# Kernel optimization log

Measured on AMD Instinct MI355X. Metric: run time of the kernel, lower is better.

## Reference

```python
import jax, jax.numpy as jnp
import numpy as np

N_NODES = 100000

def setup_inputs() -> dict:
    key = jax.random.key(0)
    k1, k2, k3, k4, k5 = jax.random.split(key, 5)
    E = 1600000
    feat = jax.random.normal(k1, (N_NODES, 128), dtype=jnp.float32)
    W = jax.random.normal(k2, (128, 32), dtype=jnp.float32) * 0.08  # ~xavier scale
    edge_w = jax.random.uniform(k3, (E,), dtype=jnp.float32)
    src = jax.random.randint(k4, (E,), 0, N_NODES, dtype=jnp.int32)
    dst = jax.random.randint(k5, (E,), 0, N_NODES, dtype=jnp.int32)
    return {"feat": feat, "W": W, "edge_w": edge_w, "src": src, "dst": dst}

def reference(feat, W, edge_w, src, dst):
    # linear transform: [N, in] @ [in, out] -> [N, out]
    h = feat @ W
    # gather source features per edge, scale by edge weight: u_mul_e
    m = h[src] * edge_w[:, None]  # [E, out]
    # sum messages at destination nodes
    rst = jax.ops.segment_sum(m, dst, num_segments=N_NODES)  # [N, out]
    return rst
```

## Files before the change

kernel.cpp:

```cpp
#include <hip/hip_runtime.h>
#include <hip/hip_fp16.h>

constexpr int N_IN    = 128;
constexpr int N_OUT   = 32;
constexpr int LOG_R   = 6;
constexpr int RANGE   = 1 << LOG_R;
constexpr int MAXNB   = 2048;
constexpr int NCC     = 256;
constexpr int PBLK    = 512;
constexpr int CHUNK_P = 2048;

union H4 { uint2 u; __half2 h2[2]; };
union H8 { uint4 u; __half2 h2[4]; };

__global__ __launch_bounds__(256) void gemm_h(
    const float* __restrict__ feat, const float* __restrict__ W,
    __half* __restrict__ h, int n)
{
    __shared__ float Ws[N_IN * N_OUT];
    for (int i = threadIdx.x; i < (N_IN * N_OUT) / 4; i += 256)
        reinterpret_cast<float4*>(Ws)[i] = reinterpret_cast<const float4*>(W)[i];
    __syncthreads();

    int gid = blockIdx.x * 256 + threadIdx.x;
    int row = gid >> 3;
    if (row >= n) return;
    int cg = (gid & 7) * 4;

    const float4* frow = reinterpret_cast<const float4*>(feat + (size_t)row * N_IN);
    float4 acc = make_float4(0.f, 0.f, 0.f, 0.f);
    #pragma unroll
    for (int k4 = 0; k4 < N_IN / 4; ++k4) {
        float4 f = frow[k4];
        int k = k4 * 4;
        float4 w0 = *reinterpret_cast<const float4*>(&Ws[(k + 0) * N_OUT + cg]);
        float4 w1 = *reinterpret_cast<const float4*>(&Ws[(k + 1) * N_OUT + cg]);
        float4 w2 = *reinterpret_cast<const float4*>(&Ws[(k + 2) * N_OUT + cg]);
        float4 w3 = *reinterpret_cast<const float4*>(&Ws[(k + 3) * N_OUT + cg]);
        acc.x += f.x * w0.x + f.y * w1.x + f.z * w2.x + f.w * w3.x;
        acc.y += f.x * w0.y + f.y * w1.y + f.z * w2.y + f.w * w3.y;
        acc.z += f.x * w0.z + f.y * w1.z + f.z * w2.z + f.w * w3.z;
        acc.w += f.x * w0.w + f.y * w1.w + f.z * w2.w + f.w * w3.w;
    }
    H4 v;
    v.h2[0] = __float22half2_rn(make_float2(acc.x, acc.y));
    v.h2[1] = __float22half2_rn(make_float2(acc.z, acc.w));
    *reinterpret_cast<uint2*>(h + (size_t)row * N_OUT + cg) = v.u;
}

__global__ __launch_bounds__(PBLK) void partition2_k(
    const int* __restrict__ src, const int* __restrict__ dst,
    const float* __restrict__ w, int* __restrict__ tbl,
    int2* __restrict__ sw, int E, int NB, int epc)
{
    __shared__ int hist[MAXNB];
    __shared__ int wscan[PBLK];

    const int c   = blockIdx.x;
    const int tid = threadIdx.x;
    const int e0  = c * epc;
    const int e1  = min(e0 + epc, E);
    const int m   = max(e1 - e0, 0);
    const int m4  = m & ~3;
    const int slots = (NB + PBLK - 1) / PBLK;

    for (int i = tid; i < NB; i += PBLK) hist[i] = 0;
    __syncthreads();

    for (int o = tid * 4; o < m4; o += PBLK * 4) {
        int4 dv = *reinterpret_cast<const int4*>(dst + e0 + o);
        atomicAdd(&hist[dv.x >> LOG_R], 1);
        atomicAdd(&hist[dv.y >> LOG_R], 1);
        atomicAdd(&hist[dv.z >> LOG_R], 1);
        atomicAdd(&hist[dv.w >> LOG_R], 1);
    }
    if (m4 + tid < m) atomicAdd(&hist[dst[e0 + m4 + tid] >> LOG_R], 1);
    __syncthreads();

    int tsum = 0;
    int base = tid * slots;
    for (int j = 0; j < slots; ++j) {
        int idx = base + j;
        if (idx < NB) tsum += hist[idx];
    }
    wscan[tid] = tsum;
    __syncthreads();
    for (int off = 1; off < PBLK; off <<= 1) {
        int x = (tid >= off) ? wscan[tid - off] : 0;
        __syncthreads();
        wscan[tid] += x;
        __syncthreads();
    }
    int run = wscan[tid] - tsum;
    __syncthreads();
    for (int j = 0; j < slots; ++j) {
        int idx = base + j;
        if (idx < NB) {
            int cval = hist[idx];
            tbl[(size_t)c * (NB + 1) + idx] = run;
            hist[idx] = run;
            run += cval;
        }
    }
    if (tid == 0) tbl[(size_t)c * (NB + 1) + NB] = m;
    __syncthreads();

    int2* outp = sw + (size_t)c * epc;
    for (int o = tid * 4; o < m4; o += PBLK * 4) {
        int4   sv = *reinterpret_cast<const int4*>(src + e0 + o);
        int4   dv = *reinterpret_cast<const int4*>(dst + e0 + o);
        float4 wv = *reinterpret_cast<const float4*>(w + e0 + o);
        int p0 = atomicAdd(&hist[dv.x >> LOG_R], 1);
        int p1 = atomicAdd(&hist[dv.y >> LOG_R], 1);
        int p2 = atomicAdd(&hist[dv.z >> LOG_R], 1);
        int p3 = atomicAdd(&hist[dv.w >> LOG_R], 1);
        outp[p0] = make_int2(sv.x | ((dv.x & (RANGE - 1)) << 17), __float_as_int(wv.x));
        outp[p1] = make_int2(sv.y | ((dv.y & (RANGE - 1)) << 17), __float_as_int(wv.y));
        outp[p2] = make_int2(sv.z | ((dv.z & (RANGE - 1)) << 17), __float_as_int(wv.z));
        outp[p3] = make_int2(sv.w | ((dv.w & (RANGE - 1)) << 17), __float_as_int(wv.w));
    }
    if (m4 + tid < m) {
        int e = e0 + m4 + tid;
        int d = dst[e];
        int pos = atomicAdd(&hist[d >> LOG_R], 1);
        outp[pos] = make_int2(src[e] | ((d & (RANGE - 1)) << 17), __float_as_int(w[e]));
    }
}

__global__ __launch_bounds__(256) void conv6_k(
    const __half* __restrict__ h, const int2* __restrict__ sw,
    const int* __restrict__ tbl, float* __restrict__ out,
    int n, int NB, int ncc, int epc)
{
    __shared__ int2 pairs[CHUNK_P];
    __shared__ unsigned short order[CHUNK_P];
    __shared__ int cnt[RANGE];
    __shared__ int sc[RANGE];
    __shared__ int start[RANGE + 1];
    __shared__ int cur[RANGE];
    __shared__ int rs[NCC];
    __shared__ int ps[NCC + 1];
    __shared__ int stmp[256];

    const int b    = blockIdx.x;
    const int tid  = threadIdx.x;
    const int node = tid >> 2;
    const int cg8  = (tid & 3) * 8;

    int len = 0;
    if (tid < ncc) {
        int s0 = tbl[(size_t)tid * (NB + 1) + b];
        int s1 = tbl[(size_t)tid * (NB + 1) + b + 1];
        rs[tid] = s0;
        len = s1 - s0;
    }
    stmp[tid] = len;
    __syncthreads();
    for (int off = 1; off < 256; off <<= 1) {
        int x = (tid >= off) ? stmp[tid - off] : 0;
        __syncthreads();
        stmp[tid] += x;
        __syncthreads();
    }
    ps[tid + 1] = stmp[tid];
    if (tid == 0) ps[0] = 0;
    __syncthreads();
    const int deg = ps[ncc];

    float4 acc01 = make_float4(0.f, 0.f, 0.f, 0.f);
    float4 acc23 = make_float4(0.f, 0.f, 0.f, 0.f);

    #define GLOAD(p, f0, f1, f2, f3)                                           \
        H8 _x##f0;                                                             \
        _x##f0.u = *reinterpret_cast<const uint4*>(                            \
            h + (size_t)((p).x & 0x1FFFF) * N_OUT + cg8);                      \
        float2 f0 = __half22float2(_x##f0.h2[0]);                              \
        float2 f1 = __half22float2(_x##f0.h2[1]);                              \
        float2 f2 = __half22float2(_x##f0.h2[2]);                              \
        float2 f3 = __half22float2(_x##f0.h2[3]);
    #define GACC(p, f0, f1, f2, f3)                                            \
    {                                                                          \
        float wv = __int_as_float((p).y);                                      \
        acc01.x += f0.x * wv; acc01.y += f0.y * wv;                            \
        acc01.z += f1.x * wv; acc01.w += f1.y * wv;                            \
        acc23.x += f2.x * wv; acc23.y += f2.y * wv;                            \
        acc23.z += f3.x * wv; acc23.w += f3.y * wv;                            \
    }

    if (deg <= CHUNK_P) {
        if (tid < RANGE) cnt[tid] = 0;
        __syncthreads();

        {
            int d0 = ps[tid];
            int l  = ps[tid + 1] - d0;
            const int2* sp = sw + (size_t)tid * epc + rs[tid];
            for (int j = 0; j < l; ++j) {
                int2 p = sp[j];
                pairs[d0 + j] = p;
                atomicAdd(&cnt[p.x >> 17], 1);
            }
        }
        __syncthreads();

        int v = 0;
        if (tid < RANGE) { v = cnt[tid]; sc[tid] = v; }
        __syncthreads();
        #pragma unroll
        for (int off = 1; off < RANGE; off <<= 1) {
            int x = (tid < RANGE && tid >= off) ? sc[tid - off] : 0;
            __syncthreads();
            if (tid < RANGE) sc[tid] += x;
            __syncthreads();
        }
        if (tid < RANGE) { start[tid] = sc[tid] - v; cur[tid] = sc[tid] - v; }
        if (tid == RANGE - 1) start[RANGE] = sc[RANGE - 1];
        __syncthreads();

        for (int i = tid; i < deg; i += 256) {
            int loc = pairs[i].x >> 17;
            int pos = atomicAdd(&cur[loc], 1);
            order[pos] = (unsigned short)i;
        }
        __syncthreads();

        int k  = start[node];
        int ke = start[node + 1];
        for (; k + 3 < ke; k += 4) {
            int2 p0 = pairs[order[k + 0]], p1 = pairs[order[k + 1]];
            int2 p2 = pairs[order[k + 2]], p3 = pairs[order[k + 3]];
            GLOAD(p0, a0, a1, a2, a3)
            GLOAD(p1, b0, b1, b2, b3)
            GLOAD(p2, c0, c1, c2, c3)
            GLOAD(p3, d0, d1, d2, d3)
            GACC(p0, a0, a1, a2, a3)
            GACC(p1, b0, b1, b2, b3)
            GACC(p2, c0, c1, c2, c3)
            GACC(p3, d0, d1, d2, d3)
        }
        for (; k < ke; ++k) {
            int2 p = pairs[order[k]];
            GLOAD(p, e0, e1, e2, e3)
            GACC(p, e0, e1, e2, e3)
        }
    } else {
        for (int cbase = 0; cbase < deg; cbase += CHUNK_P) {
            const int m = min(CHUNK_P, deg - cbase);
            for (int i = tid; i < m; i += 256) {
                int gidx = cbase + i;
                int lo = 0, hi = ncc - 1;
                while (lo < hi) {
                    int mid = (lo + hi + 1) >> 1;
                    if (ps[mid] <= gidx) lo = mid; else hi = mid - 1;
                }
                int off = gidx - ps[lo];
                pairs[i] = sw[(size_t)lo * epc + rs[lo] + off];
            }
            __syncthreads();
            for (int k = 0; k < m; ++k) {
                int2 p = pairs[k];
                if ((p.x >> 17) == node) {
                    GLOAD(p, f0, f1, f2, f3)
                    GACC(p, f0, f1, f2, f3)
                }
            }
            __syncthreads();
        }
    }
    #undef GLOAD
    #undef GACC

    int node0 = b * RANGE + node;
    if (node0 < n) {
        float* o = out + (size_t)node0 * N_OUT + cg8;
        *reinterpret_cast<float4*>(o + 0) = acc01;
        *reinterpret_cast<float4*>(o + 4) = acc23;
    }
}

__global__ __launch_bounds__(256) void fused_edge(
    const float* __restrict__ feat, const float* __restrict__ W,
    const float* __restrict__ edge_w, const int* __restrict__ src,
    const int* __restrict__ dst, float* __restrict__ out, int E)
{
    __shared__ float Ws[N_IN * N_OUT];
    for (int i = threadIdx.x; i < (N_IN * N_OUT) / 4; i += 256)
        reinterpret_cast<float4*>(Ws)[i] = reinterpret_cast<const float4*>(W)[i];
    __syncthreads();
    int gid = blockIdx.x * 256 + threadIdx.x;
    int e = gid >> 3;
    if (e >= E) return;
    int cg = (gid & 7) * 4;
    int s = src[e];
    int d = dst[e];
    float w = edge_w[e];
    const float4* frow = reinterpret_cast<const float4*>(feat + (size_t)s * N_IN);
    float4 acc = make_float4(0.f, 0.f, 0.f, 0.f);
    #pragma unroll
    for (int k4 = 0; k4 < N_IN / 4; ++k4) {
        float4 f = frow[k4];
        int k = k4 * 4;
        float4 w0 = *reinterpret_cast<const float4*>(&Ws[(k + 0) * N_OUT + cg]);
        float4 w1 = *reinterpret_cast<const float4*>(&Ws[(k + 1) * N_OUT + cg]);
        float4 w2 = *reinterpret_cast<const float4*>(&Ws[(k + 2) * N_OUT + cg]);
        float4 w3 = *reinterpret_cast<const float4*>(&Ws[(k + 3) * N_OUT + cg]);
        acc.x += f.x * w0.x + f.y * w1.x + f.z * w2.x + f.w * w3.x;
        acc.y += f.x * w0.y + f.y * w1.y + f.z * w2.y + f.w * w3.y;
        acc.z += f.x * w0.z + f.y * w1.z + f.z * w2.z + f.w * w3.z;
        acc.w += f.x * w0.w + f.y * w1.w + f.z * w2.w + f.w * w3.w;
    }
    float* o = out + (size_t)d * N_OUT + cg;
    atomicAdd(o + 0, acc.x * w);
    atomicAdd(o + 1, acc.y * w);
    atomicAdd(o + 2, acc.z * w);
    atomicAdd(o + 3, acc.w * w);
}

extern "C" void kernel_launch(void* const* d_in, const int* in_sizes, int n_in,
                              void* d_out, int out_size, void* d_ws, size_t ws_size,
                              hipStream_t stream) {
    const float* feat   = (const float*)d_in[0];
    const float* W      = (const float*)d_in[1];
    const float* edge_w = (const float*)d_in[2];
    const int*   src    = (const int*)d_in[3];
    const int*   dst    = (const int*)d_in[4];
    float* out = (float*)d_out;

    int n = in_sizes[0] / N_IN;
    int E = in_sizes[2];

    int NB  = (n + RANGE - 1) / RANGE;
    int ncc = NCC;
    int epc = (((E + ncc - 1) / ncc) + 3) & ~3;

    size_t off_h   = 0;
    size_t off_tbl = (off_h + (size_t)n * N_OUT * sizeof(__half) + 15) & ~(size_t)15;
    size_t off_sw  = (off_tbl + (size_t)ncc * (NB + 1) * sizeof(int) + 15) & ~(size_t)15;
    size_t need    = off_sw + (size_t)ncc * epc * sizeof(int2);

    bool ok = (ws_size >= need) && (n <= (1 << 17)) && (NB <= MAXNB);

    if (ok) {
        char* ws = (char*)d_ws;
        __half* h  = (__half*)(ws + off_h);
        int*   tbl = (int*)(ws + off_tbl);
        int2*  sw  = (int2*)(ws + off_sw);

        long gthreads = (long)n * 8;
        gemm_h<<<(int)((gthreads + 255) / 256), 256, 0, stream>>>(feat, W, h, n);
        partition2_k<<<ncc, PBLK, 0, stream>>>(src, dst, edge_w, tbl, sw, E, NB, epc);
        conv6_k<<<NB, 256, 0, stream>>>(h, sw, tbl, out, n, NB, ncc, epc);
    } else {
        hipError_t _e = hipMemsetAsync(d_out, 0, (size_t)out_size * sizeof(float), stream);
        (void)_e;
        long sthreads = (long)E * 8;
        fused_edge<<<(int)((sthreads + 255) / 256), 256, 0, stream>>>(feat, W, edge_w, src, dst, out, E);
    }
}
```

Before: 76.35 us.

## Merge GEMM and edge partition into one launch, unroll gather by eight

```diff
diff --git a/kernel.cpp b/kernel.cpp
--- a/kernel.cpp
+++ b/kernel.cpp
@@ -7,123 +7,124 @@
 constexpr int RANGE   = 1 << LOG_R;
 constexpr int MAXNB   = 2048;
 constexpr int NCC     = 256;
-constexpr int PBLK    = 512;
+constexpr int FBLK    = 512;
 constexpr int CHUNK_P = 2048;
 
 union H4 { uint2 u; __half2 h2[2]; };
 union H8 { uint4 u; __half2 h2[4]; };
 
-__global__ __launch_bounds__(256) void gemm_h(
+__global__ __launch_bounds__(FBLK) void gemm_part_k(
     const float* __restrict__ feat, const float* __restrict__ W,
-    __half* __restrict__ h, int n)
+    const int* __restrict__ src, const int* __restrict__ dst,
+    const float* __restrict__ ew, __half* __restrict__ h,
+    int* __restrict__ tbl, int2* __restrict__ sw,
+    int n, int E, int NB, int epc, int ncc)
 {
-    __shared__ float Ws[N_IN * N_OUT];
-    for (int i = threadIdx.x; i < (N_IN * N_OUT) / 4; i += 256)
-        reinterpret_cast<float4*>(Ws)[i] = reinterpret_cast<const float4*>(W)[i];
-    __syncthreads();
-
-    int gid = blockIdx.x * 256 + threadIdx.x;
-    int row = gid >> 3;
-    if (row >= n) return;
-    int cg = (gid & 7) * 4;
-
-    const float4* frow = reinterpret_cast<const float4*>(feat + (size_t)row * N_IN);
-    float4 acc = make_float4(0.f, 0.f, 0.f, 0.f);
-    #pragma unroll
-    for (int k4 = 0; k4 < N_IN / 4; ++k4) {
-        float4 f = frow[k4];
-        int k = k4 * 4;
-        float4 w0 = *reinterpret_cast<const float4*>(&Ws[(k + 0) * N_OUT + cg]);
-        float4 w1 = *reinterpret_cast<const float4*>(&Ws[(k + 1) * N_OUT + cg]);
-        float4 w2 = *reinterpret_cast<const float4*>(&Ws[(k + 2) * N_OUT + cg]);
-        float4 w3 = *reinterpret_cast<const float4*>(&Ws[(k + 3) * N_OUT + cg]);
-        acc.x += f.x * w0.x + f.y * w1.x + f.z * w2.x + f.w * w3.x;
-        acc.y += f.x * w0.y + f.y * w1.y + f.z * w2.y + f.w * w3.y;
-        acc.z += f.x * w0.z + f.y * w1.z + f.z * w2.z + f.w * w3.z;
-        acc.w += f.x * w0.w + f.y * w1.w + f.z * w2.w + f.w * w3.w;
-    }
-    H4 v;
-    v.h2[0] = __float22half2_rn(make_float2(acc.x, acc.y));
-    v.h2[1] = __float22half2_rn(make_float2(acc.z, acc.w));
-    *reinterpret_cast<uint2*>(h + (size_t)row * N_OUT + cg) = v.u;
-}
-
-__global__ __launch_bounds__(PBLK) void partition2_k(
-    const int* __restrict__ src, const int* __restrict__ dst,
-    const float* __restrict__ w, int* __restrict__ tbl,
-    int2* __restrict__ sw, int E, int NB, int epc)
-{
-    __shared__ int hist[MAXNB];
-    __shared__ int wscan[PBLK];
-
-    const int c   = blockIdx.x;
+    __shared__ __align__(16) char smem[N_IN * N_OUT * sizeof(float)];
     const int tid = threadIdx.x;
-    const int e0  = c * epc;
-    const int e1  = min(e0 + epc, E);
-    const int m   = max(e1 - e0, 0);
-    const int m4  = m & ~3;
-    const int slots = (NB + PBLK - 1) / PBLK;
-
-    for (int i = tid; i < NB; i += PBLK) hist[i] = 0;
-    __syncthreads();
-
-    for (int o = tid * 4; o < m4; o += PBLK * 4) {
-        int4 dv = *reinterpret_cast<const int4*>(dst + e0 + o);
-        atomicAdd(&hist[dv.x >> LOG_R], 1);
-        atomicAdd(&hist[dv.y >> LOG_R], 1);
-        atomicAdd(&hist[dv.z >> LOG_R], 1);
-        atomicAdd(&hist[dv.w >> LOG_R], 1);
-    }
-    if (m4 + tid < m) atomicAdd(&hist[dst[e0 + m4 + tid] >> LOG_R], 1);
-    __syncthreads();
-
-    int tsum = 0;
-    int base = tid * slots;
-    for (int j = 0; j < slots; ++j) {
-        int idx = base + j;
-        if (idx < NB) tsum += hist[idx];
-    }
-    wscan[tid] = tsum;
-    __syncthreads();
-    for (int off = 1; off < PBLK; off <<= 1) {
-        int x = (tid >= off) ? wscan[tid - off] : 0;
-        __syncthreads();
-        wscan[tid] += x;
-        __syncthreads();
-    }
-    int run = wscan[tid] - tsum;
-    __syncthreads();
-    for (int j = 0; j < slots; ++j) {
-        int idx = base + j;
-        if (idx < NB) {
-            int cval = hist[idx];
-            tbl[(size_t)c * (NB + 1) + idx] = run;
-            hist[idx] = run;
-            run += cval;
-        }
-    }
-    if (tid == 0) tbl[(size_t)c * (NB + 1) + NB] = m;
-    __syncthreads();
-
-    int2* outp = sw + (size_t)c * epc;
-    for (int o = tid * 4; o < m4; o += PBLK * 4) {
-        int4   sv = *reinterpret_cast<const int4*>(src + e0 + o);
-        int4   dv = *reinterpret_cast<const int4*>(dst + e0 + o);
-        float4 wv = *reinterpret_cast<const float4*>(w + e0 + o);
-        int p0 = atomicAdd(&hist[dv.x >> LOG_R], 1);
-        int p1 = atomicAdd(&hist[dv.y >> LOG_R], 1);
-        int p2 = atomicAdd(&hist[dv.z >> LOG_R], 1);
-        int p3 = atomicAdd(&hist[dv.w >> LOG_R], 1);
-        outp[p0] = make_int2(sv.x | ((dv.x & (RANGE - 1)) << 17), __float_as_int(wv.x));
-        outp[p1] = make_int2(sv.y | ((dv.y & (RANGE - 1)) << 17), __float_as_int(wv.y));
-        outp[p2] = make_int2(sv.z | ((dv.z & (RANGE - 1)) << 17), __float_as_int(wv.z));
-        outp[p3] = make_int2(sv.w | ((dv.w & (RANGE - 1)) << 17), __float_as_int(wv.w));
-    }
-    if (m4 + tid < m) {
-        int e = e0 + m4 + tid;
-        int d = dst[e];
-        int pos = atomicAdd(&hist[d >> LOG_R], 1);
-        outp[pos] = make_int2(src[e] | ((d & (RANGE - 1)) << 17), __float_as_int(w[e]));
+
+    if ((int)blockIdx.x < ncc) {
+        int* hist  = (int*)smem;
+        int* wscan = (int*)(smem + MAXNB * 4);
+
+        const int c   = blockIdx.x;
+        const int e0  = c * epc;
+        const int e1  = min(e0 + epc, E);
+        const int m   = max(e1 - e0, 0);
+        const int m4  = m & ~3;
+        const int slots = (NB + FBLK - 1) / FBLK;
+
+        for (int i = tid; i < NB; i += FBLK) hist[i] = 0;
+        __syncthreads();
+
+        for (int o = tid * 4; o < m4; o += FBLK * 4) {
+            int4 dv = *reinterpret_cast<const int4*>(dst + e0 + o);
+            atomicAdd(&hist[dv.x >> LOG_R], 1);
+            atomicAdd(&hist[dv.y >> LOG_R], 1);
+            atomicAdd(&hist[dv.z >> LOG_R], 1);
+            atomicAdd(&hist[dv.w >> LOG_R], 1);
+        }
+        if (m4 + tid < m) atomicAdd(&hist[dst[e0 + m4 + tid] >> LOG_R], 1);
+        __syncthreads();
+
+        int tsum = 0;
+        int base = tid * slots;
+        for (int j = 0; j < slots; ++j) {
+            int idx = base + j;
+            if (idx < NB) tsum += hist[idx];
+        }
+        wscan[tid] = tsum;
+        __syncthreads();
+        for (int off = 1; off < FBLK; off <<= 1) {
+            int x = (tid >= off) ? wscan[tid - off] : 0;
+            __syncthreads();
+            wscan[tid] += x;
+            __syncthreads();
+        }
+        int run = wscan[tid] - tsum;
+        __syncthreads();
+        for (int j = 0; j < slots; ++j) {
+            int idx = base + j;
+            if (idx < NB) {
+                int cval = hist[idx];
+                tbl[(size_t)c * (NB + 1) + idx] = run;
+                hist[idx] = run;
+                run += cval;
+            }
+        }
+        if (tid == 0) tbl[(size_t)c * (NB + 1) + NB] = m;
+        __syncthreads();
+
+        int2* outp = sw + (size_t)c * epc;
+        for (int o = tid * 4; o < m4; o += FBLK * 4) {
+            int4   sv = *reinterpret_cast<const int4*>(src + e0 + o);
+            int4   dv = *reinterpret_cast<const int4*>(dst + e0 + o);
+            float4 wv = *reinterpret_cast<const float4*>(ew + e0 + o);
+            int p0 = atomicAdd(&hist[dv.x >> LOG_R], 1);
+            int p1 = atomicAdd(&hist[dv.y >> LOG_R], 1);
+            int p2 = atomicAdd(&hist[dv.z >> LOG_R], 1);
+            int p3 = atomicAdd(&hist[dv.w >> LOG_R], 1);
+            outp[p0] = make_int2(sv.x | ((dv.x & (RANGE - 1)) << 17), __float_as_int(wv.x));
+            outp[p1] = make_int2(sv.y | ((dv.y & (RANGE - 1)) << 17), __float_as_int(wv.y));
+            outp[p2] = make_int2(sv.z | ((dv.z & (RANGE - 1)) << 17), __float_as_int(wv.z));
+            outp[p3] = make_int2(sv.w | ((dv.w & (RANGE - 1)) << 17), __float_as_int(wv.w));
+        }
+        if (m4 + tid < m) {
+            int e = e0 + m4 + tid;
+            int d = dst[e];
+            int pos = atomicAdd(&hist[d >> LOG_R], 1);
+            outp[pos] = make_int2(src[e] | ((d & (RANGE - 1)) << 17), __float_as_int(ew[e]));
+        }
+    } else {
+        float* Ws = (float*)smem;
+        for (int i = tid; i < (N_IN * N_OUT) / 4; i += FBLK)
+            reinterpret_cast<float4*>(Ws)[i] = reinterpret_cast<const float4*>(W)[i];
+        __syncthreads();
+
+        int gid = ((int)blockIdx.x - ncc) * FBLK + tid;
+        int row = gid >> 3;
+        if (row >= n) return;
+        int cg = (gid & 7) * 4;
+
+        const float4* frow = reinterpret_cast<const float4*>(feat + (size_t)row * N_IN);
+        float4 acc = make_float4(0.f, 0.f, 0.f, 0.f);
+        #pragma unroll
+        for (int k4 = 0; k4 < N_IN / 4; ++k4) {
+            float4 f = frow[k4];
+            int k = k4 * 4;
+            float4 w0 = *reinterpret_cast<const float4*>(&Ws[(k + 0) * N_OUT + cg]);
+            float4 w1 = *reinterpret_cast<const float4*>(&Ws[(k + 1) * N_OUT + cg]);
+            float4 w2 = *reinterpret_cast<const float4*>(&Ws[(k + 2) * N_OUT + cg]);
+            float4 w3 = *reinterpret_cast<const float4*>(&Ws[(k + 3) * N_OUT + cg]);
+            acc.x += f.x * w0.x + f.y * w1.x + f.z * w2.x + f.w * w3.x;
+            acc.y += f.x * w0.y + f.y * w1.y + f.z * w2.y + f.w * w3.y;
+            acc.z += f.x * w0.z + f.y * w1.z + f.z * w2.z + f.w * w3.z;
+            acc.w += f.x * w0.w + f.y * w1.w + f.z * w2.w + f.w * w3.w;
+        }
+        H4 v;
+        v.h2[0] = __float22half2_rn(make_float2(acc.x, acc.y));
+        v.h2[1] = __float22half2_rn(make_float2(acc.z, acc.w));
+        *reinterpret_cast<uint2*>(h + (size_t)row * N_OUT + cg) = v.u;
     }
 }
 
@@ -226,22 +227,44 @@
 
         int k  = start[node];
         int ke = start[node + 1];
+        for (; k + 7 < ke; k += 8) {
+            int2 q0 = pairs[order[k + 0]], q1 = pairs[order[k + 1]];
+            int2 q2 = pairs[order[k + 2]], q3 = pairs[order[k + 3]];
+            int2 q4 = pairs[order[k + 4]], q5 = pairs[order[k + 5]];
+            int2 q6 = pairs[order[k + 6]], q7 = pairs[order[k + 7]];
+            GLOAD(q0, m0, m1, m2, m3)
+            GLOAD(q1, n0, n1, n2, n3)
+            GLOAD(q2, o0, o1, o2, o3)
+            GLOAD(q3, p0, p1, p2, p3)
+            GLOAD(q4, r0, r1, r2, r3)
+            GLOAD(q5, s0, s1, s2, s3)
+            GLOAD(q6, t0, t1, t2, t3)
+            GLOAD(q7, u0, u1, u2, u3)
+            GACC(q0, m0, m1, m2, m3)
+            GACC(q1, n0, n1, n2, n3)
+            GACC(q2, o0, o1, o2, o3)
+            GACC(q3, p0, p1, p2, p3)
+            GACC(q4, r0, r1, r2, r3)
+            GACC(q5, s0, s1, s2, s3)
+            GACC(q6, t0, t1, t2, t3)
+            GACC(q7, u0, u1, u2, u3)
+        }
         for (; k + 3 < ke; k += 4) {
-            int2 p0 = pairs[order[k + 0]], p1 = pairs[order[k + 1]];
-            int2 p2 = pairs[order[k + 2]], p3 = pairs[order[k + 3]];
-            GLOAD(p0, a0, a1, a2, a3)
-            GLOAD(p1, b0, b1, b2, b3)
-            GLOAD(p2, c0, c1, c2, c3)
-            GLOAD(p3, d0, d1, d2, d3)
-            GACC(p0, a0, a1, a2, a3)
-            GACC(p1, b0, b1, b2, b3)
-            GACC(p2, c0, c1, c2, c3)
-            GACC(p3, d0, d1, d2, d3)
+            int2 q0 = pairs[order[k + 0]], q1 = pairs[order[k + 1]];
+            int2 q2 = pairs[order[k + 2]], q3 = pairs[order[k + 3]];
+            GLOAD(q0, a0, a1, a2, a3)
+            GLOAD(q1, b0, b1, b2, b3)
+            GLOAD(q2, c0, c1, c2, c3)
+            GLOAD(q3, d0, d1, d2, d3)
+            GACC(q0, a0, a1, a2, a3)
+            GACC(q1, b0, b1, b2, b3)
+            GACC(q2, c0, c1, c2, c3)
+            GACC(q3, d0, d1, d2, d3)
         }
         for (; k < ke; ++k) {
-            int2 p = pairs[order[k]];
-            GLOAD(p, e0, e1, e2, e3)
-            GACC(p, e0, e1, e2, e3)
+            int2 q = pairs[order[k]];
+            GLOAD(q, e0, e1, e2, e3)
+            GACC(q, e0, e1, e2, e3)
         }
     } else {
         for (int cbase = 0; cbase < deg; cbase += CHUNK_P) {
@@ -346,9 +369,9 @@
         int*   tbl = (int*)(ws + off_tbl);
         int2*  sw  = (int2*)(ws + off_sw);
 
-        long gthreads = (long)n * 8;
-        gemm_h<<<(int)((gthreads + 255) / 256), 256, 0, stream>>>(feat, W, h, n);
-        partition2_k<<<ncc, PBLK, 0, stream>>>(src, dst, edge_w, tbl, sw, E, NB, epc);
+        int gemm_blocks = (int)(((long)n * 8 + FBLK - 1) / FBLK);
+        gemm_part_k<<<ncc + gemm_blocks, FBLK, 0, stream>>>(
+            feat, W, src, dst, edge_w, h, tbl, sw, n, E, NB, epc, ncc);
         conv6_k<<<NB, 256, 0, stream>>>(h, sw, tbl, out, n, NB, ncc, epc);
     } else {
         hipError_t _e = hipMemsetAsync(d_out, 0, (size_t)out_size * sizeof(float), stream);
```

New measurement: 71.71 us, median of 2. 6.1% less time.
